# Kernel tuning notes

Hardware: AMD Instinct MI355X
Metric: run time of the kernel (lower is better)

Reference implementation:

```python
import jax, jax.numpy as jnp
import numpy as np

N_SAMPLES = 64
N_AGENTS = 64          # agents per sample (fully connected subgraph)
N = N_SAMPLES * N_AGENTS
F_DIM = 128            # decoder_latent_size
EDIM = 2
ZDIM = 2 * F_DIM + EDIM
BN_EPS = 1e-5


def _build_edge_index():
    # fully-connected (no self loops) per sample, with node offsets, COO row-major
    idx = np.arange(N_AGENTS)
    rows = np.repeat(idx, N_AGENTS)
    cols = np.tile(idx, N_AGENTS)
    mask = rows != cols
    rows, cols = rows[mask], cols[mask]
    offs = (np.arange(N_SAMPLES) * N_AGENTS)[:, None]
    src = (rows[None, :] + offs).ravel().astype(np.int32)  # edge_index[0] = source j
    dst = (cols[None, :] + offs).ravel().astype(np.int32)  # edge_index[1] = target i
    return src, dst


def setup_inputs() -> dict:
    key = jax.random.key(0)
    ks = jax.random.split(key, 12)
    src, dst = _build_edge_index()
    s = 1.0 / np.sqrt(ZDIM)
    inp = {
        "gnn_in": jax.random.normal(ks[0], (N, F_DIM), dtype=jnp.float32),
        "centers": jax.random.normal(ks[1], (N, EDIM), dtype=jnp.float32),
        "src": jnp.asarray(src),
        "dst": jnp.asarray(dst),
        "Wf1": jax.random.normal(ks[2], (F_DIM, ZDIM), dtype=jnp.float32) * s,
        "bf1": jnp.zeros((F_DIM,), jnp.float32),
        "Ws1": jax.random.normal(ks[3], (F_DIM, ZDIM), dtype=jnp.float32) * s,
        "bs1": jnp.zeros((F_DIM,), jnp.float32),
        "g1": jnp.ones((F_DIM,), jnp.float32),
        "be1": jnp.zeros((F_DIM,), jnp.float32),
        "Wf2": jax.random.normal(ks[4], (F_DIM, ZDIM), dtype=jnp.float32) * s,
        "bf2": jnp.zeros((F_DIM,), jnp.float32),
        "Ws2": jax.random.normal(ks[5], (F_DIM, ZDIM), dtype=jnp.float32) * s,
        "bs2": jnp.zeros((F_DIM,), jnp.float32),
        "g2": jnp.ones((F_DIM,), jnp.float32),
        "be2": jnp.zeros((F_DIM,), jnp.float32),
    }
    return inp


def _cgconv(x, edge_attr, src, dst, Wf, bf, Ws, bs, gamma, beta):
    # z_ij = [x_i, x_j, e_ij]  (i = target = dst, j = source = src)
    z = jnp.concatenate([x[dst], x[src], edge_attr], axis=-1)        # [E, 2F+2]
    msg = jax.nn.sigmoid(z @ Wf.T + bf) * jax.nn.softplus(z @ Ws.T + bs)  # [E, F]
    agg = jax.ops.segment_sum(msg, dst, num_segments=N)              # [N, F]
    # BatchNorm1d (training mode: batch stats, biased var), then residual
    mean = agg.mean(axis=0)
    var = agg.var(axis=0)
    agg = (agg - mean) * jax.lax.rsqrt(var + BN_EPS) * gamma + beta
    return agg + x


def reference(gnn_in, centers, src, dst,
              Wf1, bf1, Ws1, bs1, g1, be1,
              Wf2, bf2, Ws2, bs2, g2, be2):
    edge_attr = centers[dst] - centers[src]                           # data[cols] - data[rows]
    x = jax.nn.relu(_cgconv(gnn_in, edge_attr, src, dst, Wf1, bf1, Ws1, bs1, g1, be1))
    out = jax.nn.relu(_cgconv(x, edge_attr, src, dst, Wf2, bf2, Ws2, bs2, g2, be2))
    # original splits per sample; uniform sample size -> concatenation == out itself
    return out
```

## Files before the change

kernel.cpp:

```cpp
#include <hip/hip_runtime.h>

constexpr int NS = 64;
constexpr int NA = 64;
constexpr int NN = NS * NA;
constexpr int FD = 128;
constexpr int ZD = 2 * FD + 2;
constexpr int FS = 16;
constexpr int NB = NS * (FD / FS);
constexpr int NT = 512;
constexpr int XPAD = 132;
constexpr float BN_EPS = 1e-5f;
constexpr float L2E = 1.44269504088896f;
constexpr float LN2 = 0.69314718055995f;

__device__ __forceinline__ void stage_w(
    float4 (*wlds)[FS], const float* __restrict__ Wf, const float* __restrict__ Ws,
    int fq, int tid)
{
    for (int i = tid; i < FD * FS; i += NT) {
        int k = i >> 4, fr = i & (FS - 1);
        int row = (fq * FS + fr) * ZD;
        wlds[k][fr] = make_float4(Wf[row + k], Wf[row + FD + k],
                                  Ws[row + k], Ws[row + FD + k]);
    }
}

__device__ __forceinline__ void layer_tail(
    float aPf0, float aQf0, float aPs0, float aQs0,
    float aPf1, float aQf1, float aPs1, float aQs1,
    const float2* cs, float2 (*q)[FS],
    const float* __restrict__ Wf, const float* __restrict__ Ws,
    const float* __restrict__ bf, const float* __restrict__ bs,
    int tid, int fl, int ig, int f, int s, int fq, int base,
    float* __restrict__ agg, float* __restrict__ pS, float* __restrict__ pSS,
    float& aOut0, float& aOut1)
{
    float we0 = Wf[f*ZD + 2*FD], we1 = Wf[f*ZD + 2*FD + 1];
    float ws0 = Ws[f*ZD + 2*FD], ws1 = Ws[f*ZD + 2*FD + 1];
    float bfv = bf[f], bsv = bs[f];
    float2 c0 = cs[ig], c1 = cs[ig + 32];
    float cf0 = c0.x*we0 + c0.y*we1, cg0 = c0.x*ws0 + c0.y*ws1;
    float cf1 = c1.x*we0 + c1.y*we1, cg1 = c1.x*ws0 + c1.y*ws1;
    float Pf0 = aPf0 + cf0 + bfv, Ps0 = aPs0 + cg0 + bsv;
    float Pf1 = aPf1 + cf1 + bfv, Ps1 = aPs1 + cg1 + bsv;
    float Qf0 = aQf0 - cf0,       Qs0 = aQs0 - cg0;
    float Qf1 = aQf1 - cf1,       Qs1 = aQs1 - cg1;
    float2 p0 = make_float2(__builtin_amdgcn_exp2f(-Pf0*L2E), __builtin_amdgcn_exp2f(Ps0*L2E));
    float2 p1 = make_float2(__builtin_amdgcn_exp2f(-Pf1*L2E), __builtin_amdgcn_exp2f(Ps1*L2E));
    q[ig][fl]    = make_float2(__builtin_amdgcn_exp2f(-Qf0*L2E), __builtin_amdgcn_exp2f(Qs0*L2E));
    q[ig+32][fl] = make_float2(__builtin_amdgcn_exp2f(-Qf1*L2E), __builtin_amdgcn_exp2f(Qs1*L2E));
    __syncthreads();

    float a0=0.f, a1=0.f, b0=0.f, b1=0.f;
    #pragma unroll 4
    for (int j = 0; j < NA; j += 2) {
        float2 qa = q[j][fl];
        float2 qb = q[j+1][fl];
        a0 = fmaf(__builtin_amdgcn_rcpf(1.0f + p0.x*qa.x),
                  __builtin_amdgcn_logf(1.0f + p0.y*qa.y), a0);
        b0 = fmaf(__builtin_amdgcn_rcpf(1.0f + p1.x*qa.x),
                  __builtin_amdgcn_logf(1.0f + p1.y*qa.y), b0);
        a1 = fmaf(__builtin_amdgcn_rcpf(1.0f + p0.x*qb.x),
                  __builtin_amdgcn_logf(1.0f + p0.y*qb.y), a1);
        b1 = fmaf(__builtin_amdgcn_rcpf(1.0f + p1.x*qb.x),
                  __builtin_amdgcn_logf(1.0f + p1.y*qb.y), b1);
    }
    float aA = a0 + a1, aB = b0 + b1;
    {
        float2 qv0 = q[ig][fl];
        aA -= __builtin_amdgcn_rcpf(1.0f + p0.x*qv0.x) *
              __builtin_amdgcn_logf(1.0f + p0.y*qv0.y);
        float2 qv1 = q[ig+32][fl];
        aB -= __builtin_amdgcn_rcpf(1.0f + p1.x*qv1.x) *
              __builtin_amdgcn_logf(1.0f + p1.y*qv1.y);
    }
    aA *= LN2; aB *= LN2;
    agg[(base + ig) * FD + f]      = aA;
    agg[(base + ig + 32) * FD + f] = aB;

    __syncthreads();
    float* sm = (float*)q;
    sm[tid]      = aA + aB;
    sm[NT + tid] = aA*aA + aB*aB;
    __syncthreads();
    if (tid < FS) {
        float sv = 0.f, qv = 0.f;
        #pragma unroll
        for (int r = 0; r < 32; ++r) {
            sv += sm[r * FS + tid];
            qv += sm[NT + r * FS + tid];
        }
        pS [s * FD + fq * FS + tid] = sv;
        pSS[s * FD + fq * FS + tid] = qv;
    }
    aOut0 = aA; aOut1 = aB;
}

#define GEMM_STEP(xv, wv) \
    aPf0 = fmaf(x0.xv, wv.x, aPf0); aQf0 = fmaf(x0.xv, wv.y, aQf0); \
    aPs0 = fmaf(x0.xv, wv.z, aPs0); aQs0 = fmaf(x0.xv, wv.w, aQs0); \
    aPf1 = fmaf(x1.xv, wv.x, aPf1); aQf1 = fmaf(x1.xv, wv.y, aQf1); \
    aPs1 = fmaf(x1.xv, wv.z, aPs1); aQs1 = fmaf(x1.xv, wv.w, aQs1);

__global__ __launch_bounds__(NT) void layer1_kernel(
    const float* __restrict__ X0, const float* __restrict__ C,
    const float* __restrict__ Wf, const float* __restrict__ Ws,
    const float* __restrict__ bf, const float* __restrict__ bs,
    const float* __restrict__ Wf2, const float* __restrict__ Ws2,
    float4* __restrict__ PK2,
    float* __restrict__ agg, float* __restrict__ pS, float* __restrict__ pSS)
{
    __shared__ __align__(16) float xs[NA][XPAD];
    __shared__ float4 wlds[FD][FS];
    __shared__ float2 q[NA][FS];
    __shared__ float2 cs[NA];
    int tid = threadIdx.x, bid = blockIdx.x;
    int s = bid & (NS - 1), fq = bid >> 6;
    int base = s * NA;
    if (s == 0) {
        for (int i = tid; i < FD * FS; i += NT) {
            int k = i >> 4, fr = i & (FS - 1);
            int f2 = fq * FS + fr;
            PK2[k * FD + f2] = make_float4(Wf2[f2*ZD+k], Wf2[f2*ZD+FD+k],
                                           Ws2[f2*ZD+k], Ws2[f2*ZD+FD+k]);
        }
    }
    stage_w(wlds, Wf, Ws, fq, tid);
    const float4* Xv = (const float4*)(X0 + base * FD);
    for (int idx = tid; idx < NA * FD / 4; idx += NT) {
        int n = idx >> 5, k4 = idx & 31;
        *(float4*)&xs[n][k4 * 4] = Xv[idx];
    }
    if (tid < NA) cs[tid] = ((const float2*)C)[base + tid];
    __syncthreads();

    const int fl = tid & (FS - 1), ig = tid >> 4;
    const int f  = fq * FS + fl;
    float aPf0=0.f,aQf0=0.f,aPs0=0.f,aQs0=0.f;
    float aPf1=0.f,aQf1=0.f,aPs1=0.f,aQs1=0.f;
    #pragma unroll 2
    for (int k = 0; k < FD; k += 4) {
        float4 x0 = *(const float4*)&xs[ig][k];
        float4 x1 = *(const float4*)&xs[ig + 32][k];
        float4 w0 = wlds[k + 0][fl];
        float4 w1 = wlds[k + 1][fl];
        float4 w2 = wlds[k + 2][fl];
        float4 w3 = wlds[k + 3][fl];
        GEMM_STEP(x, w0) GEMM_STEP(y, w1) GEMM_STEP(z, w2) GEMM_STEP(w, w3)
    }
    float d0, d1;
    layer_tail(aPf0,aQf0,aPs0,aQs0, aPf1,aQf1,aPs1,aQs1,
               cs, q, Wf, Ws, bf, bs, tid, fl, ig, f, s, fq, base,
               agg, pS, pSS, d0, d1);
}

__global__ __launch_bounds__(NT) void layer2_kernel(
    const float* __restrict__ X0, const float* __restrict__ agg1,
    const float* __restrict__ C,
    const float* __restrict__ pS1, const float* __restrict__ pSS1,
    const float* __restrict__ g1, const float* __restrict__ be1,
    const float* __restrict__ Wf, const float* __restrict__ Ws,
    const float* __restrict__ bf, const float* __restrict__ bs,
    const float4* __restrict__ PK2,
    float* __restrict__ x1, float* __restrict__ agg2,
    float* __restrict__ pS2, float* __restrict__ pSS2)
{
    __shared__ __align__(16) float xs[NA][XPAD];
    __shared__ float2 q[NA][FS];
    __shared__ float2 cs[NA];
    __shared__ float bnsc[FD], bnsh[FD];
    int tid = threadIdx.x, bid = blockIdx.x;
    int s = bid & (NS - 1), fq = bid >> 6;
    int base = s * NA;
    {
        int fr = tid & (FD - 1), sq = tid >> 7;
        float sv = 0.f, qv = 0.f;
        #pragma unroll
        for (int s2 = 0; s2 < NS / 4; ++s2) {
            int si = sq * (NS / 4) + s2;
            sv += pS1[si * FD + fr];
            qv += pSS1[si * FD + fr];
        }
        float* sm = (float*)q;
        sm[tid] = sv;
        sm[NT + tid] = qv;
    }
    if (tid < NA) cs[tid] = ((const float2*)C)[base + tid];
    __syncthreads();
    if (tid < FD) {
        const float* sm = (const float*)q;
        float sv = sm[tid] + sm[FD + tid] + sm[2*FD + tid] + sm[3*FD + tid];
        float qv = sm[NT + tid] + sm[NT + FD + tid] + sm[NT + 2*FD + tid] + sm[NT + 3*FD + tid];
        float m  = sv * (1.0f / NN);
        float v  = qv * (1.0f / NN) - m * m;
        float sc = g1[tid] * rsqrtf(v + BN_EPS);
        bnsc[tid] = sc;
        bnsh[tid] = be1[tid] - m * sc;
    }
    __syncthreads();
    const float4* Xv  = (const float4*)(X0 + base * FD);
    const float4* Av  = (const float4*)(agg1 + base * FD);
    float4*       X1v = (float4*)(x1 + base * FD);
    for (int idx = tid; idx < NA * FD / 4; idx += NT) {
        int n = idx >> 5, k4 = (idx & 31) * 4;
        float4 x = Xv[idx], a = Av[idx];
        float4 r;
        r.x = fmaxf(fmaf(a.x, bnsc[k4 + 0], bnsh[k4 + 0]) + x.x, 0.0f);
        r.y = fmaxf(fmaf(a.y, bnsc[k4 + 1], bnsh[k4 + 1]) + x.y, 0.0f);
        r.z = fmaxf(fmaf(a.z, bnsc[k4 + 2], bnsh[k4 + 2]) + x.z, 0.0f);
        r.w = fmaxf(fmaf(a.w, bnsc[k4 + 3], bnsh[k4 + 3]) + x.w, 0.0f);
        *(float4*)&xs[n][k4] = r;
        X1v[idx] = r;
    }
    __syncthreads();

    const int fl = tid & (FS - 1), ig = tid >> 4;
    const int f  = fq * FS + fl;
    const float4* Wp = PK2 + f;
    float aPf0=0.f,aQf0=0.f,aPs0=0.f,aQs0=0.f;
    float aPf1=0.f,aQf1=0.f,aPs1=0.f,aQs1=0.f;
    #pragma unroll 2
    for (int k = 0; k < FD; k += 4) {
        float4 x0 = *(const float4*)&xs[ig][k];
        float4 x1v = *(const float4*)&xs[ig + 32][k];
        float4 w0 = Wp[(k + 0) * FD];
        float4 w1 = Wp[(k + 1) * FD];
        float4 w2 = Wp[(k + 2) * FD];
        float4 w3 = Wp[(k + 3) * FD];
        float4 x1 = x1v;
        GEMM_STEP(x, w0) GEMM_STEP(y, w1) GEMM_STEP(z, w2) GEMM_STEP(w, w3)
    }
    float d0, d1;
    layer_tail(aPf0,aQf0,aPs0,aQs0, aPf1,aQf1,aPs1,aQs1,
               cs, q, Wf, Ws, bf, bs, tid, fl, ig, f, s, fq, base,
               agg2, pS2, pSS2, d0, d1);
}

__global__ __launch_bounds__(256) void out_kernel(
    const float4* __restrict__ x1, const float4* __restrict__ agg2,
    const float* __restrict__ pS2, const float* __restrict__ pSS2,
    const float* __restrict__ g2, const float* __restrict__ be2,
    float4* __restrict__ out)
{
    __shared__ float sm[1024];
    __shared__ float sc[FD], sh[FD];
    int tid = threadIdx.x;
    {
        int fr = tid & (FD - 1), sq = tid >> 7;
        float sv = 0.f, qv = 0.f;
        #pragma unroll
        for (int s2 = 0; s2 < NS / 2; ++s2) {
            int si = sq * (NS / 2) + s2;
            sv += pS2[si * FD + fr];
            qv += pSS2[si * FD + fr];
        }
        sm[tid] = sv;
        sm[512 + tid] = qv;
    }
    __syncthreads();
    if (tid < FD) {
        float sv = sm[tid] + sm[FD + tid];
        float qv = sm[512 + tid] + sm[512 + FD + tid];
        float m  = sv * (1.0f / NN);
        float v  = qv * (1.0f / NN) - m * m;
        float scl = g2[tid] * rsqrtf(v + BN_EPS);
        sc[tid] = scl;
        sh[tid] = be2[tid] - m * scl;
    }
    __syncthreads();
    int idx = blockIdx.x * 256 + tid;
    int f0 = (idx & 31) * 4;
    float4 xv = x1[idx], av = agg2[idx];
    float4 r;
    r.x = fmaxf(fmaf(av.x, sc[f0 + 0], sh[f0 + 0]) + xv.x, 0.0f);
    r.y = fmaxf(fmaf(av.y, sc[f0 + 1], sh[f0 + 1]) + xv.y, 0.0f);
    r.z = fmaxf(fmaf(av.z, sc[f0 + 2], sh[f0 + 2]) + xv.z, 0.0f);
    r.w = fmaxf(fmaf(av.w, sc[f0 + 3], sh[f0 + 3]) + xv.w, 0.0f);
    out[idx] = r;
}

extern "C" void kernel_launch(void* const* d_in, const int* in_sizes, int n_in,
                              void* d_out, int out_size, void* d_ws, size_t ws_size,
                              hipStream_t stream) {
    const float* gnn_in  = (const float*)d_in[0];
    const float* centers = (const float*)d_in[1];
    const float* Wf1 = (const float*)d_in[4];
    const float* bf1 = (const float*)d_in[5];
    const float* Ws1 = (const float*)d_in[6];
    const float* bs1 = (const float*)d_in[7];
    const float* g1  = (const float*)d_in[8];
    const float* be1 = (const float*)d_in[9];
    const float* Wf2 = (const float*)d_in[10];
    const float* bf2 = (const float*)d_in[11];
    const float* Ws2 = (const float*)d_in[12];
    const float* bs2 = (const float*)d_in[13];
    const float* g2  = (const float*)d_in[14];
    const float* be2 = (const float*)d_in[15];

    char* ws = (char*)d_ws;
    float*  agg1 = (float*)(ws);
    float*  agg2 = (float*)(ws + (2 << 20));
    float*  x1   = (float*)(ws + (4 << 20));
    float*  p1S  = (float*)(ws + (6 << 20));
    float*  p1SS = (float*)(ws + (6 << 20) + (32 << 10));
    float*  p2S  = (float*)(ws + (6 << 20) + (64 << 10));
    float*  p2SS = (float*)(ws + (6 << 20) + (96 << 10));
    float4* PK2  = (float4*)(ws + (6 << 20) + (128 << 10));

    layer1_kernel<<<NB, NT, 0, stream>>>(gnn_in, centers, Wf1, Ws1, bf1, bs1,
                                         Wf2, Ws2, PK2, agg1, p1S, p1SS);
    layer2_kernel<<<NB, NT, 0, stream>>>(gnn_in, agg1, centers, p1S, p1SS, g1, be1,
                                         Wf2, Ws2, bf2, bs2, PK2,
                                         x1, agg2, p2S, p2SS);
    out_kernel<<<NN * FD / 4 / 256, 256, 0, stream>>>(
        (const float4*)x1, (const float4*)agg2, p2S, p2SS, g2, be2, (float4*)d_out);
}
```

Baseline: 138.3 us.

## Pack both layers' weights in a separate kernel and read them from global memory

```diff
diff --git a/kernel.cpp b/kernel.cpp
--- a/kernel.cpp
+++ b/kernel.cpp
@@ -13,16 +13,17 @@
 constexpr float L2E = 1.44269504088896f;
 constexpr float LN2 = 0.69314718055995f;
 
-__device__ __forceinline__ void stage_w(
-    float4 (*wlds)[FS], const float* __restrict__ Wf, const float* __restrict__ Ws,
-    int fq, int tid)
-{
-    for (int i = tid; i < FD * FS; i += NT) {
-        int k = i >> 4, fr = i & (FS - 1);
-        int row = (fq * FS + fr) * ZD;
-        wlds[k][fr] = make_float4(Wf[row + k], Wf[row + FD + k],
-                                  Ws[row + k], Ws[row + FD + k]);
-    }
+__global__ __launch_bounds__(256) void pack_kernel(
+    const float* __restrict__ Wf1, const float* __restrict__ Ws1, float4* __restrict__ PK1,
+    const float* __restrict__ Wf2, const float* __restrict__ Ws2, float4* __restrict__ PK2)
+{
+    int gidx = blockIdx.x * 256 + threadIdx.x;
+    const float* Wf; const float* Ws; float4* PK; int i;
+    if (gidx < FD * FD) { Wf = Wf1; Ws = Ws1; PK = PK1; i = gidx; }
+    else                { Wf = Wf2; Ws = Ws2; PK = PK2; i = gidx - FD * FD; }
+    int k = i >> 7, f = i & 127;
+    PK[i] = make_float4(Wf[f * ZD + k], Wf[f * ZD + FD + k],
+                        Ws[f * ZD + k], Ws[f * ZD + FD + k]);
 }
 
 __device__ __forceinline__ void layer_tail(
@@ -32,8 +33,7 @@
     const float* __restrict__ Wf, const float* __restrict__ Ws,
     const float* __restrict__ bf, const float* __restrict__ bs,
     int tid, int fl, int ig, int f, int s, int fq, int base,
-    float* __restrict__ agg, float* __restrict__ pS, float* __restrict__ pSS,
-    float& aOut0, float& aOut1)
+    float* __restrict__ agg, float* __restrict__ pS, float* __restrict__ pSS)
 {
     float we0 = Wf[f*ZD + 2*FD], we1 = Wf[f*ZD + 2*FD + 1];
     float ws0 = Ws[f*ZD + 2*FD], ws1 = Ws[f*ZD + 2*FD + 1];
@@ -93,7 +93,6 @@
         pS [s * FD + fq * FS + tid] = sv;
         pSS[s * FD + fq * FS + tid] = qv;
     }
-    aOut0 = aA; aOut1 = aB;
 }
 
 #define GEMM_STEP(xv, wv) \
@@ -102,30 +101,34 @@
     aPf1 = fmaf(x1.xv, wv.x, aPf1); aQf1 = fmaf(x1.xv, wv.y, aQf1); \
     aPs1 = fmaf(x1.xv, wv.z, aPs1); aQs1 = fmaf(x1.xv, wv.w, aQs1);
 
-__global__ __launch_bounds__(NT) void layer1_kernel(
+#define GEMM_LOOP(PKp) \
+    float aPf0=0.f,aQf0=0.f,aPs0=0.f,aQs0=0.f; \
+    float aPf1=0.f,aQf1=0.f,aPs1=0.f,aQs1=0.f; \
+    { const float4* Wp = (PKp) + f; \
+      _Pragma("unroll 2") \
+      for (int k = 0; k < FD; k += 4) { \
+        float4 x0 = *(const float4*)&xs[ig][k]; \
+        float4 x1 = *(const float4*)&xs[ig + 32][k]; \
+        float4 w0 = Wp[(k + 0) * FD]; \
+        float4 w1 = Wp[(k + 1) * FD]; \
+        float4 w2 = Wp[(k + 2) * FD]; \
+        float4 w3 = Wp[(k + 3) * FD]; \
+        GEMM_STEP(x, w0) GEMM_STEP(y, w1) GEMM_STEP(z, w2) GEMM_STEP(w, w3) \
+      } }
+
+__global__ __launch_bounds__(NT, 6) void layer1_kernel(
     const float* __restrict__ X0, const float* __restrict__ C,
+    const float4* __restrict__ PK,
     const float* __restrict__ Wf, const float* __restrict__ Ws,
     const float* __restrict__ bf, const float* __restrict__ bs,
-    const float* __restrict__ Wf2, const float* __restrict__ Ws2,
-    float4* __restrict__ PK2,
     float* __restrict__ agg, float* __restrict__ pS, float* __restrict__ pSS)
 {
     __shared__ __align__(16) float xs[NA][XPAD];
-    __shared__ float4 wlds[FD][FS];
     __shared__ float2 q[NA][FS];
     __shared__ float2 cs[NA];
     int tid = threadIdx.x, bid = blockIdx.x;
     int s = bid & (NS - 1), fq = bid >> 6;
     int base = s * NA;
-    if (s == 0) {
-        for (int i = tid; i < FD * FS; i += NT) {
-            int k = i >> 4, fr = i & (FS - 1);
-            int f2 = fq * FS + fr;
-            PK2[k * FD + f2] = make_float4(Wf2[f2*ZD+k], Wf2[f2*ZD+FD+k],
-                                           Ws2[f2*ZD+k], Ws2[f2*ZD+FD+k]);
-        }
-    }
-    stage_w(wlds, Wf, Ws, fq, tid);
     const float4* Xv = (const float4*)(X0 + base * FD);
     for (int idx = tid; idx < NA * FD / 4; idx += NT) {
         int n = idx >> 5, k4 = idx & 31;
@@ -133,35 +136,21 @@
     }
     if (tid < NA) cs[tid] = ((const float2*)C)[base + tid];
     __syncthreads();
-
     const int fl = tid & (FS - 1), ig = tid >> 4;
     const int f  = fq * FS + fl;
-    float aPf0=0.f,aQf0=0.f,aPs0=0.f,aQs0=0.f;
-    float aPf1=0.f,aQf1=0.f,aPs1=0.f,aQs1=0.f;
-    #pragma unroll 2
-    for (int k = 0; k < FD; k += 4) {
-        float4 x0 = *(const float4*)&xs[ig][k];
-        float4 x1 = *(const float4*)&xs[ig + 32][k];
-        float4 w0 = wlds[k + 0][fl];
-        float4 w1 = wlds[k + 1][fl];
-        float4 w2 = wlds[k + 2][fl];
-        float4 w3 = wlds[k + 3][fl];
-        GEMM_STEP(x, w0) GEMM_STEP(y, w1) GEMM_STEP(z, w2) GEMM_STEP(w, w3)
-    }
-    float d0, d1;
+    GEMM_LOOP(PK)
     layer_tail(aPf0,aQf0,aPs0,aQs0, aPf1,aQf1,aPs1,aQs1,
-               cs, q, Wf, Ws, bf, bs, tid, fl, ig, f, s, fq, base,
-               agg, pS, pSS, d0, d1);
-}
-
-__global__ __launch_bounds__(NT) void layer2_kernel(
+               cs, q, Wf, Ws, bf, bs, tid, fl, ig, f, s, fq, base, agg, pS, pSS);
+}
+
+__global__ __launch_bounds__(NT, 6) void layer2_kernel(
     const float* __restrict__ X0, const float* __restrict__ agg1,
     const float* __restrict__ C,
     const float* __restrict__ pS1, const float* __restrict__ pSS1,
     const float* __restrict__ g1, const float* __restrict__ be1,
+    const float4* __restrict__ PK,
     const float* __restrict__ Wf, const float* __restrict__ Ws,
     const float* __restrict__ bf, const float* __restrict__ bs,
-    const float4* __restrict__ PK2,
     float* __restrict__ x1, float* __restrict__ agg2,
     float* __restrict__ pS2, float* __restrict__ pSS2)
 {
@@ -213,27 +202,11 @@
         X1v[idx] = r;
     }
     __syncthreads();
-
     const int fl = tid & (FS - 1), ig = tid >> 4;
     const int f  = fq * FS + fl;
-    const float4* Wp = PK2 + f;
-    float aPf0=0.f,aQf0=0.f,aPs0=0.f,aQs0=0.f;
-    float aPf1=0.f,aQf1=0.f,aPs1=0.f,aQs1=0.f;
-    #pragma unroll 2
-    for (int k = 0; k < FD; k += 4) {
-        float4 x0 = *(const float4*)&xs[ig][k];
-        float4 x1v = *(const float4*)&xs[ig + 32][k];
-        float4 w0 = Wp[(k + 0) * FD];
-        float4 w1 = Wp[(k + 1) * FD];
-        float4 w2 = Wp[(k + 2) * FD];
-        float4 w3 = Wp[(k + 3) * FD];
-        float4 x1 = x1v;
-        GEMM_STEP(x, w0) GEMM_STEP(y, w1) GEMM_STEP(z, w2) GEMM_STEP(w, w3)
-    }
-    float d0, d1;
+    GEMM_LOOP(PK)
     layer_tail(aPf0,aQf0,aPs0,aQs0, aPf1,aQf1,aPs1,aQs1,
-               cs, q, Wf, Ws, bf, bs, tid, fl, ig, f, s, fq, base,
-               agg2, pS2, pSS2, d0, d1);
+               cs, q, Wf, Ws, bf, bs, tid, fl, ig, f, s, fq, base, agg2, pS2, pSS2);
 }
 
 __global__ __launch_bounds__(256) void out_kernel(
@@ -305,12 +278,14 @@
     float*  p1SS = (float*)(ws + (6 << 20) + (32 << 10));
     float*  p2S  = (float*)(ws + (6 << 20) + (64 << 10));
     float*  p2SS = (float*)(ws + (6 << 20) + (96 << 10));
-    float4* PK2  = (float4*)(ws + (6 << 20) + (128 << 10));
-
-    layer1_kernel<<<NB, NT, 0, stream>>>(gnn_in, centers, Wf1, Ws1, bf1, bs1,
-                                         Wf2, Ws2, PK2, agg1, p1S, p1SS);
+    float4* PK1  = (float4*)(ws + (6 << 20) + (128 << 10));
+    float4* PK2  = (float4*)(ws + (6 << 20) + (384 << 10));
+
+    pack_kernel<<<128, 256, 0, stream>>>(Wf1, Ws1, PK1, Wf2, Ws2, PK2);
+    layer1_kernel<<<NB, NT, 0, stream>>>(gnn_in, centers, PK1, Wf1, Ws1, bf1, bs1,
+                                         agg1, p1S, p1SS);
     layer2_kernel<<<NB, NT, 0, stream>>>(gnn_in, agg1, centers, p1S, p1SS, g1, be1,
-                                         Wf2, Ws2, bf2, bs2, PK2,
+                                         PK2, Wf2, Ws2, bf2, bs2,
                                          x1, agg2, p2S, p2SS);
     out_kernel<<<NN * FD / 4 / 256, 256, 0, stream>>>(
         (const float4*)x1, (const float4*)agg2, p2S, p2SS, g2, be2, (float4*)d_out);
```

Result: no change. 140.6 us (+1.6%).
